# Kernel optimization log

Measured on AMD Instinct MI355X. Metric: run time of the kernel, lower is better.

The kernel has to match this reference:

```python
import jax, jax.numpy as jnp
import numpy as np
from jax import lax

# Module constants (from init_kwargs)
IN_FEATURES = 4096
OUT_FEATURES = 11008
TD_X = 16
TD_Y = 16
IN_PART = (2048, 2048)
L = 16
KV = (4, 4)
V = 2
TLUT_BITS = 9


def _decode_trellis(trellis, tlut, m, k_part, kv):
    """Bitshift-trellis decode of a compressed weight partition.

    trellis: [nb, nw] int32 holding 16-bit words (nb = (m/td_x)*(k_part/td_y)).
    Each step consumes kv bits, updating an L-bit sliding state; the low
    tlut_bits of the state index the LUT, yielding V weights per step.
    Returns dense weights [m, k_part].
    """
    nb, nw = trellis.shape
    steps = (TD_X * TD_Y) // V  # codes per block
    cpw = 16 // kv  # chunks per 16-bit word (kv divides 16)
    words = trellis.astype(jnp.int32) & 0xFFFF
    shifts = 16 - kv * (jnp.arange(cpw, dtype=jnp.int32) + 1)  # big-endian in word
    chunks = (words[:, :, None] >> shifts[None, None, :]) & ((1 << kv) - 1)
    chunks = chunks.reshape(nb, nw * cpw)[:, :steps]  # [nb, steps]

    l_mask = (1 << L) - 1
    t_mask = (1 << TLUT_BITS) - 1

    def step(state, c):
        state = ((state << kv) | c) & l_mask
        return state, state & t_mask

    _, idx = lax.scan(step, jnp.zeros((nb,), jnp.int32), chunks.T)  # [steps, nb]
    vals = tlut[idx]  # [steps, nb, V]
    blocks = vals.transpose(1, 0, 2).reshape(nb, TD_X, TD_Y)
    mo, ko = m // TD_X, k_part // TD_Y
    return blocks.reshape(mo, ko, TD_X, TD_Y).transpose(0, 2, 1, 3).reshape(m, k_part)


def setup_inputs() -> dict:
    key = jax.random.key(0)
    k1, k2, k3, k4 = jax.random.split(key, 4)
    nb = (OUT_FEATURES // TD_X) * (IN_PART[0] // TD_Y)
    nw = (TD_X * TD_Y * KV[0]) // 16 // V
    inp = jax.random.normal(k1, (4, IN_FEATURES), dtype=jnp.float32)
    trellis1 = jax.random.randint(k2, (nb, nw), 0, 65536, dtype=jnp.int32)
    trellis2 = jax.random.randint(k3, (nb, nw), 0, 65536, dtype=jnp.int32)
    tlut = jax.random.normal(k4, (2 ** TLUT_BITS, V), dtype=jnp.float32)
    return {"inp": inp, "trellis1": trellis1, "trellis2": trellis2, "tlut": tlut}


def reference(inp, trellis1, trellis2, tlut):
    x = inp.reshape(-1, IN_FEATURES)
    w1 = _decode_trellis(trellis1, tlut, OUT_FEATURES, IN_PART[0], KV[0])  # [m, k1]
    w2 = _decode_trellis(trellis2, tlut, OUT_FEATURES, IN_PART[1], KV[1])  # [m, k2]
    out = x[:, : IN_PART[0]] @ w1.T + x[:, IN_PART[0]:] @ w2.T  # [bs, m]
    return out.reshape(*inp.shape[:-1], OUT_FEATURES).astype(inp.dtype)
```

## Files before the change

### kernel.cpp

```cpp
#include <hip/hip_runtime.h>

#define IN_FEATURES 4096
#define OUT_FEATURES 11008
#define KO 128
#define NW 32
#define SEG 32
#define KO_PER_SEG (KO / SEG)
#define NPART (SEG * 2)

__global__ __launch_bounds__(256, 6) void tcq_decode_kernel(
    const float* __restrict__ inp,
    const int* __restrict__ trellis1,
    const int* __restrict__ trellis2,
    const float* __restrict__ tlut,
    float* __restrict__ ws)
{
    __shared__ float lut[1024];
    ((float4*)lut)[threadIdx.x] = ((const float4*)tlut)[threadIdx.x];
    __syncthreads();

    const int tid  = threadIdx.x;
    const int lane = tid & 63;
    const int wid  = tid >> 6;
    const int tx   = lane & 15;
    const int mt   = lane >> 4;
    const int mo   = blockIdx.x * 16 + wid * 4 + mt;
    const int m    = mo * 16 + tx;
    const int seg  = blockIdx.y;
    const int part = blockIdx.z;
    const int ko0  = seg * KO_PER_SEG;

    const int* __restrict__ tre =
        (part ? trellis2 : trellis1) + (mo * KO + ko0) * NW;
    const float* __restrict__ xk = inp + part * 2048 + ko0 * 16;

    float accE[4] = {0.f, 0.f, 0.f, 0.f};
    float accO[4] = {0.f, 0.f, 0.f, 0.f};

    #pragma unroll 1
    for (int kk = 0; kk < KO_PER_SEG; ++kk) {
        const int* blk = tre + kk * NW;
        int2 wp  = *reinterpret_cast<const int2*>(blk + 2 * tx);
        int  wm1 = tx ? blk[2 * tx - 1] : 0;
        const unsigned comb0 = (unsigned(wm1)  << 16) | (unsigned(wp.x) & 0xFFFFu);
        const unsigned comb1 = (unsigned(wp.x) << 16) | (unsigned(wp.y) & 0xFFFFu);

        float sx[4][16];
        #pragma unroll
        for (int b = 0; b < 4; ++b) {
            #pragma unroll
            for (int q = 0; q < 16; ++q)
                sx[b][q] = xk[b * IN_FEATURES + kk * 16 + q];
        }

        #pragma unroll
        for (int j = 0; j < 8; ++j) {
            const unsigned comb  = (j < 4) ? comb0 : comb1;
            const int      shift = 12 - 4 * (j & 3);
            const unsigned idx   = (comb >> shift) & 0x1FFu;
            float2 w = *reinterpret_cast<const float2*>(&lut[idx * 2]);
            #pragma unroll
            for (int b = 0; b < 4; ++b) {
                accE[b] = fmaf(w.x, sx[b][2 * j],     accE[b]);
                accO[b] = fmaf(w.y, sx[b][2 * j + 1], accO[b]);
            }
        }
    }

    float* wsp = ws + (size_t)(part * SEG + seg) * 4 * OUT_FEATURES;
    #pragma unroll
    for (int b = 0; b < 4; ++b)
        wsp[b * OUT_FEATURES + m] = accE[b] + accO[b];
}

__global__ __launch_bounds__(256) void tcq_reduce_kernel(
    const float* __restrict__ ws,
    float* __restrict__ out)
{
    const int i = blockIdx.x * 256 + threadIdx.x;
    if (i < 4 * OUT_FEATURES) {
        float s = 0.f;
        #pragma unroll
        for (int p = 0; p < NPART; ++p)
            s += ws[(size_t)p * 4 * OUT_FEATURES + i];
        out[i] = s;
    }
}

extern "C" void kernel_launch(void* const* d_in, const int* in_sizes, int n_in,
                              void* d_out, int out_size, void* d_ws, size_t ws_size,
                              hipStream_t stream) {
    const float* inp  = (const float*)d_in[0];
    const int*   t1   = (const int*)d_in[1];
    const int*   t2   = (const int*)d_in[2];
    const float* tlut = (const float*)d_in[3];
    float* out = (float*)d_out;
    float* ws  = (float*)d_ws;

    dim3 grid1(43, SEG, 2);
    hipLaunchKernelGGL(tcq_decode_kernel, grid1, dim3(256), 0, stream,
                       inp, t1, t2, tlut, ws);

    dim3 grid2((4 * OUT_FEATURES + 255) / 256);
    hipLaunchKernelGGL(tcq_reduce_kernel, grid2, dim3(256), 0, stream,
                       ws, out);
}
```

Before: 96.90 us.

## Load activations once per lane, broadcast via readlane, and prefetch next trellis block

Each lane now loads one activation element per k-block and the wavefront broadcasts values with readlane, replacing 64 uniform scalar/vector loads per thread. The previous trellis word is obtained with a cross-lane shuffle instead of a second global load, and the next block's trellis and activation loads are software-prefetched before the current block's compute. The LUT sync is moved after the initial loads so they overlap, and the occupancy hint in launch_bounds is dropped. This may change register pressure and occupancy, and readlane serializes through scalar registers.

```diff
diff --git a/kernel.cpp b/kernel.cpp
--- a/kernel.cpp
+++ b/kernel.cpp
@@ -8,7 +8,12 @@
 #define KO_PER_SEG (KO / SEG)
 #define NPART (SEG * 2)
 
-__global__ __launch_bounds__(256, 6) void tcq_decode_kernel(
+__device__ __forceinline__ float rl(float v, int l) {
+    return __builtin_bit_cast(float,
+        __builtin_amdgcn_readlane(__builtin_bit_cast(int, v), l));
+}
+
+__global__ __launch_bounds__(256) void tcq_decode_kernel(
     const float* __restrict__ inp,
     const int* __restrict__ trellis1,
     const int* __restrict__ trellis2,
@@ -17,7 +22,6 @@
 {
     __shared__ float lut[1024];
     ((float4*)lut)[threadIdx.x] = ((const float4*)tlut)[threadIdx.x];
-    __syncthreads();
 
     const int tid  = threadIdx.x;
     const int lane = tid & 63;
@@ -32,26 +36,28 @@
 
     const int* __restrict__ tre =
         (part ? trellis2 : trellis1) + (mo * KO + ko0) * NW;
-    const float* __restrict__ xk = inp + part * 2048 + ko0 * 16;
+    const float* __restrict__ xp =
+        inp + (lane >> 4) * IN_FEATURES + part * 2048 + ko0 * 16 + (lane & 15);
 
     float accE[4] = {0.f, 0.f, 0.f, 0.f};
     float accO[4] = {0.f, 0.f, 0.f, 0.f};
 
-    #pragma unroll 1
+    float xv = xp[0];
+    int2  wp = *reinterpret_cast<const int2*>(tre + 2 * tx);
+
+    __syncthreads();
+
     for (int kk = 0; kk < KO_PER_SEG; ++kk) {
-        const int* blk = tre + kk * NW;
-        int2 wp  = *reinterpret_cast<const int2*>(blk + 2 * tx);
-        int  wm1 = tx ? blk[2 * tx - 1] : 0;
+        float xv_n = 0.f; int2 wp_n = {0, 0};
+        if (kk + 1 < KO_PER_SEG) {
+            xv_n = xp[(kk + 1) * 16];
+            wp_n = *reinterpret_cast<const int2*>(tre + (kk + 1) * NW + 2 * tx);
+        }
+
+        int wm1 = __shfl_up(wp.y, 1);
+        if (tx == 0) wm1 = 0;
         const unsigned comb0 = (unsigned(wm1)  << 16) | (unsigned(wp.x) & 0xFFFFu);
         const unsigned comb1 = (unsigned(wp.x) << 16) | (unsigned(wp.y) & 0xFFFFu);
-
-        float sx[4][16];
-        #pragma unroll
-        for (int b = 0; b < 4; ++b) {
-            #pragma unroll
-            for (int q = 0; q < 16; ++q)
-                sx[b][q] = xk[b * IN_FEATURES + kk * 16 + q];
-        }
 
         #pragma unroll
         for (int j = 0; j < 8; ++j) {
@@ -61,10 +67,11 @@
             float2 w = *reinterpret_cast<const float2*>(&lut[idx * 2]);
             #pragma unroll
             for (int b = 0; b < 4; ++b) {
-                accE[b] = fmaf(w.x, sx[b][2 * j],     accE[b]);
-                accO[b] = fmaf(w.y, sx[b][2 * j + 1], accO[b]);
+                accE[b] = fmaf(w.x, rl(xv, b * 16 + 2 * j),     accE[b]);
+                accO[b] = fmaf(w.y, rl(xv, b * 16 + 2 * j + 1), accO[b]);
             }
         }
+        xv = xv_n; wp = wp_n;
     }
 
     float* wsp = ws + (size_t)(part * SEG + seg) * 4 * OUT_FEATURES;
```

Result: slower. 100.1 us (+3.3%).
